# Kernel optimization log

Hardware: AMD Instinct MI355X
Metric: run time of the kernel (lower is better)

## Reference

```python
import jax, jax.numpy as jnp
import numpy as np


def setup_inputs() -> dict:
    key = jax.random.key(0)
    ks = jax.random.split(key, 7)
    B, T, X, H, Y = 256, 2048, 64, 128, 32
    s_ih = 1.0 / np.sqrt(H)
    return {
        "x": jax.random.normal(ks[0], (B, T, X), dtype=jnp.float32),
        "W_ih": jax.random.normal(ks[1], (H, X), dtype=jnp.float32) * s_ih,
        "W_hh": jax.random.normal(ks[2], (H, H), dtype=jnp.float32) * s_ih,
        "b_ih": jax.random.normal(ks[3], (H,), dtype=jnp.float32) * s_ih,
        "b_hh": jax.random.normal(ks[4], (H,), dtype=jnp.float32) * s_ih,
        "W_out": jax.random.normal(ks[5], (Y, H), dtype=jnp.float32) * s_ih,
        "b_out": jax.random.normal(ks[6], (Y,), dtype=jnp.float32) * s_ih,
    }


def reference(x, W_ih, W_hh, b_ih, b_hh, W_out, b_out):
    # Vanilla tanh RNN (torch.nn.RNN, 1 layer, batch_first), zero initial state,
    # readout on the last timestep: h_t = tanh(x_t W_ih^T + b_ih + h_{t-1} W_hh^T + b_hh)
    B, T, X = x.shape
    H = W_hh.shape[0]
    # Precompute input projections for all timesteps in one big GEMM: [T, B, H]
    xs = (jnp.einsum('bti,hi->bth', x, W_ih) + (b_ih + b_hh)).transpose(1, 0, 2)

    def step(h, xt):
        h = jnp.tanh(xt + h @ W_hh.T)
        return h, None

    h0 = jnp.zeros((B, H), dtype=x.dtype)
    h_last, _ = jax.lax.scan(step, h0, xs)
    out = h_last @ W_out.T + b_out  # [B, Y]
    return out
```

## Files before the change

### kernel.cpp

```cpp
#include <hip/hip_runtime.h>

#define TT 2048
#define BB 256
#define XX 64
#define HH 128
#define YY 32
#define SSTR 12
#define HBUF (16 * SSTR)


typedef float v2f __attribute__((ext_vector_type(2)));
typedef float v4f __attribute__((ext_vector_type(4)));

#define PKFMA(acc, a, b)                                              \
    asm("v_pk_fma_f32 %0, %1, %2, %0 op_sel:[0,0,0] op_sel_hi:[1,1,1]"\
        : "+v"(acc) : "v"(a), "v"(b))

template<int CTRL>
static __device__ __forceinline__ float dpp_mov(float s) {
    return __int_as_float(__builtin_amdgcn_update_dpp(
        0, __float_as_int(s), CTRL, 0xF, 0xF, true));
}

static __device__ __forceinline__ void pin2(v2f& v) {
    asm volatile("" : "+v"(v));
}

static __device__ __forceinline__ void barrier_lgkm() {
    asm volatile("s_waitcnt lgkmcnt(0)" ::: "memory");
    __builtin_amdgcn_s_barrier();
    asm volatile("" ::: "memory");
}

#define LO2(v) __builtin_shufflevector(v, v, 0, 1)
#define HI2(v) __builtin_shufflevector(v, v, 2, 3)

__global__ __launch_bounds__(512)
__attribute__((amdgpu_waves_per_eu(2, 2)))
void rnn_persist_kernel(const float* __restrict__ x,
                        const float* __restrict__ W_ih,
                        const float* __restrict__ W_hh,
                        const float* __restrict__ b_ih,
                        const float* __restrict__ b_hh,
                        const float* __restrict__ W_out,
                        const float* __restrict__ b_out,
                        float* __restrict__ out)
{
    __shared__ __align__(16) float h_lds[2][HBUF];

    const int tid  = threadIdx.x;
    const int b    = blockIdx.x;
    const int w    = tid >> 6;
    const int lane = tid & 63;
    const int kg   = lane & 15;
    const int jp   = lane >> 4;
    const int j0   = (w * 4 + jp) * 4;
    const int b0   = lane & 1;
    const int b1   = (lane >> 1) & 1;
    const int o    = lane & 3;
    const int jw   = j0 + o;
    const int woff = (jw >> 3) * SSTR + (jw & 7);
    const bool writer = (lane & 12) == 0;

    const float SC = 2.8853900817779268f;

    v2f whh2[4][4];
    v2f wih2[4][2];
    #pragma unroll
    for (int jj = 0; jj < 4; ++jj) {
        const v2f* ph = (const v2f*)(W_hh + (j0 + jj) * HH + kg * 8);
        #pragma unroll
        for (int c = 0; c < 4; ++c) whh2[jj][c] = ph[c] * SC;
        const v2f* pi = (const v2f*)(W_ih + (j0 + jj) * XX + kg * 4);
        #pragma unroll
        for (int c = 0; c < 2; ++c) wih2[jj][c] = pi[c] * SC;
    }
    #pragma unroll
    for (int jj = 0; jj < 4; ++jj) {
        #pragma unroll
        for (int c = 0; c < 4; ++c) pin2(whh2[jj][c]);
        pin2(wih2[jj][0]); pin2(wih2[jj][1]);
    }
    const float bsel = (b_ih[jw] + b_hh[jw]) * SC;

    const float* xg = x + (size_t)b * TT * XX + kg * 4;

    if (tid < HBUF) h_lds[0][tid] = 0.f;

    v4f xa = *(const v4f*)xg;
    v4f xb = *(const v4f*)(xg + XX);
    __syncthreads();

#define STEP(RP, WP, XC)                                                   \
    do {                                                                   \
        const v4f* hp = (const v4f*)&h_lds[RP][kg * SSTR];                 \
        const v4f H0 = hp[0], H1 = hp[1];                                  \
        const v2f h2[4] = { LO2(H0), HI2(H0), LO2(H1), HI2(H1) };          \
        const v2f x2[2] = { LO2(XC), HI2(XC) };                            \
        float s[4];                                                        \
        _Pragma("unroll")                                                  \
        for (int jj = 0; jj < 4; ++jj) {                                   \
            v2f a = {0.f, 0.f};                                            \
            PKFMA(a, wih2[jj][0], x2[0]); PKFMA(a, wih2[jj][1], x2[1]);    \
            PKFMA(a, whh2[jj][0], h2[0]); PKFMA(a, whh2[jj][1], h2[1]);    \
            PKFMA(a, whh2[jj][2], h2[2]); PKFMA(a, whh2[jj][3], h2[3]);    \
            s[jj] = a.x + a.y;                                             \
        }                                                                  \
                           \
        float ul = b0 ? s[1] : s[0];                                       \
        float vl = b0 ? s[0] : s[1];                                       \
        ul += dpp_mov<0xB1>(vl);                                           \
        float uh = b0 ? s[3] : s[2];                                       \
        float vh = b0 ? s[2] : s[3];                                       \
        uh += dpp_mov<0xB1>(vh);                                           \
                           \
        float u  = b1 ? uh : ul;                                           \
        float vv = b1 ? ul : uh;                                           \
        u += dpp_mov<0x4E>(vv);                                            \
        \
        u += dpp_mov<0x124>(u);                             \
        u += dpp_mov<0x128>(u);                             \
        u += bsel;                          \
        const float e  = __builtin_amdgcn_exp2f(u);                        \
        const float hn = fmaf(-2.f, __builtin_amdgcn_rcpf(e + 1.f), 1.f); \
        if (writer) h_lds[WP][woff] = hn;                                  \
        barrier_lgkm();                                                    \
    } while (0)

    for (int t = 0; t < TT; t += 2) {
        STEP(0, 1, xa);
        {
            const int tn = (t + 2 < TT) ? t + 2 : TT - 1;
            xa = *(const v4f*)(xg + (size_t)tn * XX);
        }
        STEP(1, 0, xb);
        {
            const int tn = (t + 3 < TT) ? t + 3 : TT - 1;
            xb = *(const v4f*)(xg + (size_t)tn * XX);
        }
    }
#undef STEP

    if (tid < YY) {
        const float* h  = h_lds[0];
        const float* wr = W_out + tid * HH;
        float r0 = 0.f, r1 = 0.f, r2 = 0.f, r3 = 0.f;
        #pragma unroll
        for (int s16 = 0; s16 < 16; ++s16) {
            #pragma unroll
            for (int c = 0; c < 2; ++c) {
                const float4 wv = *(const float4*)(wr + s16 * 8 + c * 4);
                const float4 hv = *(const float4*)(h + s16 * SSTR + c * 4);
                r0 = fmaf(wv.x, hv.x, r0); r1 = fmaf(wv.y, hv.y, r1);
                r2 = fmaf(wv.z, hv.z, r2); r3 = fmaf(wv.w, hv.w, r3);
            }
        }
        out[b * YY + tid] = b_out[tid] + ((r0 + r1) + (r2 + r3));
    }
}

extern "C" void kernel_launch(void* const* d_in, const int* in_sizes, int n_in,
                              void* d_out, int out_size, void* d_ws, size_t ws_size,
                              hipStream_t stream) {
    const float* x     = (const float*)d_in[0];
    const float* W_ih  = (const float*)d_in[1];
    const float* W_hh  = (const float*)d_in[2];
    const float* b_ih  = (const float*)d_in[3];
    const float* b_hh  = (const float*)d_in[4];
    const float* W_out = (const float*)d_in[5];
    const float* b_out = (const float*)d_in[6];
    float* out = (float*)d_out;

    rnn_persist_kernel<<<BB, 512, 0, stream>>>(x, W_ih, W_hh, b_ih, b_hh,
                                               W_out, b_out, out);
}
```

Measured before the change: 619.1 us.

## Halve block size to 256 threads with 8-way K split per output

Each block drops from 8 to 4 waves. Every lane now covers 16 hidden inputs and 8 input features instead of 8 and 4, so the K dimension is split 8 ways and one DPP reduction stage goes away. The shared-memory h layout changes to 8 rows with stride 20, and lanes are remapped. Fewer waves should make each per-timestep barrier cheaper and shorten the cross-lane reduction, at the cost of twice the FMA work per lane on the serial critical path and more registers for the weights.

```diff
diff --git a/kernel.cpp b/kernel.cpp
--- a/kernel.cpp
+++ b/kernel.cpp
@@ -5,8 +5,8 @@
 #define XX 64
 #define HH 128
 #define YY 32
-#define SSTR 12
-#define HBUF (16 * SSTR)
+#define SSTR 20
+#define HBUF (8 * SSTR)
 
 
 typedef float v2f __attribute__((ext_vector_type(2)));
@@ -35,8 +35,8 @@
 #define LO2(v) __builtin_shufflevector(v, v, 0, 1)
 #define HI2(v) __builtin_shufflevector(v, v, 2, 3)
 
-__global__ __launch_bounds__(512)
-__attribute__((amdgpu_waves_per_eu(2, 2)))
+__global__ __launch_bounds__(256)
+__attribute__((amdgpu_waves_per_eu(1, 1)))
 void rnn_persist_kernel(const float* __restrict__ x,
                         const float* __restrict__ W_ih,
                         const float* __restrict__ W_hh,
@@ -52,91 +52,101 @@
     const int b    = blockIdx.x;
     const int w    = tid >> 6;
     const int lane = tid & 63;
-    const int kg   = lane & 15;
-    const int jp   = lane >> 4;
-    const int j0   = (w * 4 + jp) * 4;
+    const int kg   = (lane & 3) | ((lane >> 1) & 4);
+    const int jgl  = ((lane >> 2) & 1) | (((lane >> 4) & 3) << 1);
+    const int jg   = w * 8 + jgl;
+    const int j0   = jg * 4;
     const int b0   = lane & 1;
     const int b1   = (lane >> 1) & 1;
     const int o    = lane & 3;
     const int jw   = j0 + o;
-    const int woff = (jw >> 3) * SSTR + (jw & 7);
-    const bool writer = (lane & 12) == 0;
+    const int woff = (jw >> 4) * SSTR + (jw & 15);
+    const bool writer = ((lane >> 3) & 1) == 0;
 
     const float SC = 2.8853900817779268f;
 
-    v2f whh2[4][4];
-    v2f wih2[4][2];
+    v2f whh2[4][8];
+    v2f wih2[4][4];
     #pragma unroll
     for (int jj = 0; jj < 4; ++jj) {
-        const v2f* ph = (const v2f*)(W_hh + (j0 + jj) * HH + kg * 8);
+        const v2f* ph = (const v2f*)(W_hh + (j0 + jj) * HH + kg * 16);
         #pragma unroll
-        for (int c = 0; c < 4; ++c) whh2[jj][c] = ph[c] * SC;
-        const v2f* pi = (const v2f*)(W_ih + (j0 + jj) * XX + kg * 4);
+        for (int c = 0; c < 8; ++c) whh2[jj][c] = ph[c] * SC;
+        const v2f* pi = (const v2f*)(W_ih + (j0 + jj) * XX + kg * 8);
         #pragma unroll
-        for (int c = 0; c < 2; ++c) wih2[jj][c] = pi[c] * SC;
+        for (int c = 0; c < 4; ++c) wih2[jj][c] = pi[c] * SC;
     }
     #pragma unroll
     for (int jj = 0; jj < 4; ++jj) {
         #pragma unroll
-        for (int c = 0; c < 4; ++c) pin2(whh2[jj][c]);
-        pin2(wih2[jj][0]); pin2(wih2[jj][1]);
+        for (int c = 0; c < 8; ++c) pin2(whh2[jj][c]);
+        #pragma unroll
+        for (int c = 0; c < 4; ++c) pin2(wih2[jj][c]);
     }
     const float bsel = (b_ih[jw] + b_hh[jw]) * SC;
 
-    const float* xg = x + (size_t)b * TT * XX + kg * 4;
+    const float* xg = x + (size_t)b * TT * XX + kg * 8;
 
     if (tid < HBUF) h_lds[0][tid] = 0.f;
 
-    v4f xa = *(const v4f*)xg;
-    v4f xb = *(const v4f*)(xg + XX);
+    v4f xa0 = ((const v4f*)xg)[0];
+    v4f xa1 = ((const v4f*)xg)[1];
+    v4f xb0 = ((const v4f*)(xg + XX))[0];
+    v4f xb1 = ((const v4f*)(xg + XX))[1];
     __syncthreads();
 
-#define STEP(RP, WP, XC)                                                   \
+#define STEP(RP, WP, X0, X1)                                               \
     do {                                                                   \
         const v4f* hp = (const v4f*)&h_lds[RP][kg * SSTR];                 \
-        const v4f H0 = hp[0], H1 = hp[1];                                  \
-        const v2f h2[4] = { LO2(H0), HI2(H0), LO2(H1), HI2(H1) };          \
-        const v2f x2[2] = { LO2(XC), HI2(XC) };                            \
+        const v4f H0 = hp[0], H1 = hp[1], H2 = hp[2], H3 = hp[3];          \
+        const v2f x2[4] = { LO2(X0), HI2(X0), LO2(X1), HI2(X1) };          \
+        const v2f h2[8] = { LO2(H0), HI2(H0), LO2(H1), HI2(H1),            \
+                            LO2(H2), HI2(H2), LO2(H3), HI2(H3) };          \
         float s[4];                                                        \
         _Pragma("unroll")                                                  \
         for (int jj = 0; jj < 4; ++jj) {                                   \
-            v2f a = {0.f, 0.f};                                            \
-            PKFMA(a, wih2[jj][0], x2[0]); PKFMA(a, wih2[jj][1], x2[1]);    \
-            PKFMA(a, whh2[jj][0], h2[0]); PKFMA(a, whh2[jj][1], h2[1]);    \
-            PKFMA(a, whh2[jj][2], h2[2]); PKFMA(a, whh2[jj][3], h2[3]);    \
+            v2f a = {0.f, 0.f}, c = {0.f, 0.f};                            \
+            PKFMA(a, wih2[jj][0], x2[0]); PKFMA(c, wih2[jj][1], x2[1]);    \
+            PKFMA(a, wih2[jj][2], x2[2]); PKFMA(c, wih2[jj][3], x2[3]);    \
+            PKFMA(a, whh2[jj][0], h2[0]); PKFMA(c, whh2[jj][1], h2[1]);    \
+            PKFMA(a, whh2[jj][2], h2[2]); PKFMA(c, whh2[jj][3], h2[3]);    \
+            PKFMA(a, whh2[jj][4], h2[4]); PKFMA(c, whh2[jj][5], h2[5]);    \
+            PKFMA(a, whh2[jj][6], h2[6]); PKFMA(c, whh2[jj][7], h2[7]);    \
+            a = a + c;                                                     \
             s[jj] = a.x + a.y;                                             \
         }                                                                  \
-                           \
+                        \
         float ul = b0 ? s[1] : s[0];                                       \
         float vl = b0 ? s[0] : s[1];                                       \
         ul += dpp_mov<0xB1>(vl);                                           \
         float uh = b0 ? s[3] : s[2];                                       \
         float vh = b0 ? s[2] : s[3];                                       \
         uh += dpp_mov<0xB1>(vh);                                           \
-                           \
+                        \
         float u  = b1 ? uh : ul;                                           \
         float vv = b1 ? ul : uh;                                           \
         u += dpp_mov<0x4E>(vv);                                            \
-        \
-        u += dpp_mov<0x124>(u);                             \
-        u += dpp_mov<0x128>(u);                             \
+                          \
+        u += dpp_mov<0x128>(u);                                            \
         u += bsel;                          \
         const float e  = __builtin_amdgcn_exp2f(u);                        \
-        const float hn = fmaf(-2.f, __builtin_amdgcn_rcpf(e + 1.f), 1.f); \
+        const float hn = fmaf(-2.f, __builtin_amdgcn_rcpf(e + 1.f), 1.f);  \
         if (writer) h_lds[WP][woff] = hn;                                  \
         barrier_lgkm();                                                    \
     } while (0)
 
     for (int t = 0; t < TT; t += 2) {
-        STEP(0, 1, xa);
+        STEP(0, 1, xa0, xa1);
         {
             const int tn = (t + 2 < TT) ? t + 2 : TT - 1;
-            xa = *(const v4f*)(xg + (size_t)tn * XX);
+            const v4f* xp = (const v4f*)(xg + (size_t)tn * XX);
+            xa0 = xp[0]; xa1 = xp[1];
         }
-        STEP(1, 0, xb);
+        STEP(1, 0, xb0, xb1);
         {
             const int tn = (t + 3 < TT) ? t + 3 : TT - 1;
-            xb = *(const v4f*)(xg + (size_t)tn * XX);
+            const v4f* xp = (const v4f*)(xg + (size_t)tn * XX);
+            xb0 = xp[0]; xb1 = xp[1];
         }
     }
 #undef STEP
@@ -146,11 +156,11 @@
         const float* wr = W_out + tid * HH;
         float r0 = 0.f, r1 = 0.f, r2 = 0.f, r3 = 0.f;
         #pragma unroll
-        for (int s16 = 0; s16 < 16; ++s16) {
+        for (int s8 = 0; s8 < 8; ++s8) {
             #pragma unroll
-            for (int c = 0; c < 2; ++c) {
-                const float4 wv = *(const float4*)(wr + s16 * 8 + c * 4);
-                const float4 hv = *(const float4*)(h + s16 * SSTR + c * 4);
+            for (int c = 0; c < 4; ++c) {
+                const float4 wv = *(const float4*)(wr + s8 * 16 + c * 4);
+                const float4 hv = *(const float4*)(h + s8 * SSTR + c * 4);
                 r0 = fmaf(wv.x, hv.x, r0); r1 = fmaf(wv.y, hv.y, r1);
                 r2 = fmaf(wv.z, hv.z, r2); r3 = fmaf(wv.w, hv.w, r3);
             }
@@ -171,6 +181,6 @@
     const float* b_out = (const float*)d_in[6];
     float* out = (float*)d_out;
 
-    rnn_persist_kernel<<<BB, 512, 0, stream>>>(x, W_ih, W_hh, b_ih, b_hh,
+    rnn_persist_kernel<<<BB, 256, 0, stream>>>(x, W_ih, W_hh, b_ih, b_hh,
                                                W_out, b_out, out);
 }
```

After: 635.6 us. 2.7% more time.
